# Performance work log

Measured on AMD Instinct MI355X. Metric: run time of the kernel, lower is better.

## Reference

```python
import jax, jax.numpy as jnp
import numpy as np
from jax import lax

I, H, O, S = 1024, 1024, 32000, 2048


def setup_inputs() -> dict:
    key = jax.random.key(0)
    ks = jax.random.split(key, 7)
    s = 1.0 / np.sqrt(H)
    return {
        "x": jax.random.normal(ks[0], (1, S, I), jnp.float32),
        "W_ih": jax.random.uniform(ks[1], (H, I), jnp.float32, -s, s),
        "W_hh": jax.random.uniform(ks[2], (H, H), jnp.float32, -s, s),
        "b_ih": jax.random.uniform(ks[3], (H,), jnp.float32, -s, s),
        "b_hh": jax.random.uniform(ks[4], (H,), jnp.float32, -s, s),
        "W_fc": jax.random.uniform(ks[5], (O, H), jnp.float32, -s, s),
        "b_fc": jax.random.uniform(ks[6], (O,), jnp.float32, -s, s),
    }


def reference(x, W_ih, W_hh, b_ih, b_hh, W_fc, b_fc):
    # Precompute input projection for all timesteps in one GEMM: [s, H]
    xp = jnp.einsum('si,hi->sh', x[0], W_ih) + b_ih + b_hh
    h0 = jnp.zeros((W_hh.shape[0],), x.dtype)

    def step(h, xt):
        h_new = jnp.tanh(xt + h @ W_hh.T)
        return h_new, h_new

    _, hs = lax.scan(step, h0, xp)  # hs: [s, H]
    # Linear head over all timesteps: [s, O]
    return hs @ W_fc.T + b_fc
```

## Files before the change

### kernel.cpp

```cpp
#include <hip/hip_runtime.h>
#include <math.h>

typedef _Float16 f16;
typedef f16 f16x2 __attribute__((ext_vector_type(2)));
typedef f16 f16x4 __attribute__((ext_vector_type(4)));
typedef f16 f16x8 __attribute__((ext_vector_type(8)));
typedef float f32x4 __attribute__((ext_vector_type(4)));

#define HDIM 1024
#define SEQ  2048
#define NBLK 16
#define NGWK 240
#define RPB  64
#define NTIL 4000

__global__ void k_clear(unsigned long long* __restrict__ p, int n,
                        unsigned* __restrict__ summ, int ns) {
  int stride = gridDim.x * blockDim.x;
  for (int i = blockIdx.x * blockDim.x + threadIdx.x; i < n; i += stride)
    p[i] = 0ULL;
  for (int i = blockIdx.x * blockDim.x + threadIdx.x; i < ns; i += stride)
    summ[i] = 0u;
}

__global__ void k_cvt(const float* __restrict__ in, f16* __restrict__ out, int n4) {
  int stride = gridDim.x * blockDim.x;
  for (int i = blockIdx.x * blockDim.x + threadIdx.x; i < n4; i += stride) {
    float4 v = ((const float4*)in)[i];
    f16x4 o = { (f16)v.x, (f16)v.y, (f16)v.z, (f16)v.w };
    ((f16x4*)out)[i] = o;
  }
}

__global__ void k_bias(const float* __restrict__ a, const float* __restrict__ b,
                       float* __restrict__ o) {
  int i = blockIdx.x * blockDim.x + threadIdx.x;
  if (i < HDIM) o[i] = a[i] + b[i];
}

__global__ __launch_bounds__(256) void k_gemm(
    const f16* __restrict__ A, const f16* __restrict__ B,
    const float* __restrict__ bias, float* __restrict__ C, int N)
{
  const int K = 1024;
  __shared__ __align__(16) f16 lsA[128 * 32];
  __shared__ __align__(16) f16 lsB[128 * 32];
  const int tid = threadIdx.x;
  const int l   = tid & 63;
  const int wv  = tid >> 6;
  const int mb  = blockIdx.y * 128;
  const int nb  = blockIdx.x * 128;
  const int wm  = (wv >> 1) * 64;
  const int wn  = (wv & 1) * 64;

  f32x4 acc[4][4] = {};

  for (int kt = 0; kt < K; kt += 32) {
    uint4 ra[2], rb[2];
#pragma unroll
    for (int i = 0; i < 2; ++i) {
      int c = tid + i * 256;
      int row = c >> 2, off = (c & 3) * 8;
      ra[i] = *(const uint4*)(A + (size_t)(mb + row) * K + kt + off);
      rb[i] = *(const uint4*)(B + (size_t)(nb + row) * K + kt + off);
    }
    __syncthreads();
#pragma unroll
    for (int i = 0; i < 2; ++i) {
      int c = tid + i * 256;
      *(uint4*)(lsA + c * 8) = ra[i];
      *(uint4*)(lsB + c * 8) = rb[i];
    }
    __syncthreads();

    f16x8 af[4], bf[4];
#pragma unroll
    for (int m = 0; m < 4; ++m)
      af[m] = *(const f16x8*)(lsA + (wm + m * 16 + (l & 15)) * 32 + (l >> 4) * 8);
#pragma unroll
    for (int n = 0; n < 4; ++n)
      bf[n] = *(const f16x8*)(lsB + (wn + n * 16 + (l & 15)) * 32 + (l >> 4) * 8);
#pragma unroll
    for (int m = 0; m < 4; ++m)
#pragma unroll
      for (int n = 0; n < 4; ++n)
        acc[m][n] = __builtin_amdgcn_mfma_f32_16x16x32_f16(af[m], bf[n], acc[m][n], 0, 0, 0);
  }

#pragma unroll
  for (int n = 0; n < 4; ++n) {
    int col = nb + wn + n * 16 + (l & 15);
    float bv = bias[col];
#pragma unroll
    for (int m = 0; m < 4; ++m) {
#pragma unroll
      for (int j = 0; j < 4; ++j) {
        int row = mb + wm + m * 16 + (l >> 4) * 4 + j;
        C[(size_t)row * N + col] = acc[m][n][j] + bv;
      }
    }
  }
}

__device__ __forceinline__ void pub64(unsigned long long* p, unsigned long long v) {
  (void)__hip_atomic_exchange(p, v, __ATOMIC_RELAXED, __HIP_MEMORY_SCOPE_AGENT);
}
__device__ __forceinline__ void pub32(unsigned* p, unsigned v) {
  (void)__hip_atomic_exchange(p, v, __ATOMIC_RELAXED, __HIP_MEMORY_SCOPE_AGENT);
}
__device__ __forceinline__ unsigned long long rd64(const unsigned long long* p) {
  return __hip_atomic_fetch_add((unsigned long long*)p, 0ULL,
                                __ATOMIC_RELAXED, __HIP_MEMORY_SCOPE_AGENT);
}
__device__ __forceinline__ unsigned rd32(const unsigned* p) {
  return __hip_atomic_fetch_add((unsigned*)p, 0u,
                                __ATOMIC_RELAXED, __HIP_MEMORY_SCOPE_AGENT);
}

__global__ __launch_bounds__(1024, 4) void k_main(
    const float* __restrict__ W,
    const float* __restrict__ xp,
    unsigned long long* __restrict__ pairs,
    unsigned* __restrict__ summ,
    f16* __restrict__ hs,
    const f16* __restrict__ Wfc,
    const float* __restrict__ bfc,
    float* __restrict__ out)
{
  __shared__ unsigned hl[544];
  __shared__ int s_dead;
  __shared__ __align__(16) f16 lsA[128 * 32];
  __shared__ __align__(16) f16 lsB[128 * 32];

  const int tid = threadIdx.x;
  const int l   = tid & 63;
  const int wv  = tid >> 6;

  if (blockIdx.x < NBLK) {
    const int b   = blockIdx.x;
    const int w   = wv;
    const int hfl = l >> 5;
    const int ch  = l & 31;
    const int r0  = b * RPB + w * 4 + hfl * 2;
    const int c0  = ch * 32;

    if (tid == 0) s_dead = 0;

    f16x2 wv0[16], wv1[16];
    {
      const float* w0 = W + (size_t)r0 * HDIM + c0;
      const float* w1 = w0 + HDIM;
#pragma unroll
      for (int j = 0; j < 16; ++j) {
        wv0[j] = f16x2{ (f16)w0[2 * j], (f16)w0[2 * j + 1] };
        wv1[j] = f16x2{ (f16)w1[2 * j], (f16)w1[2 * j + 1] };
      }
    }

    for (unsigned t = 1; t <= SEQ; ++t) {
      float x0 = 0.f, x1 = 0.f;
      if (ch == 0) {
        const float* xr = xp + (size_t)(t - 1) * HDIM + r0;
        x0 = xr[0]; x1 = xr[1];
      }

      if (w == 0) {
        const unsigned need = t - 1;
        {
          const unsigned* sp = summ + (size_t)(t - 1) * 16 + l;
          int g = 0;
          for (;;) {
            unsigned sv = need;
            if (l < 16) sv = rd32(sp);
            if (__ballot(sv != need) == 0ULL) break;
            if (++g > (1 << 20)) { if (l == 0) s_dead = 1; break; }
          }
        }
        {
          const unsigned long long* row = pairs + (size_t)(t - 1) * 512 + l * 8;
          unsigned long long u[8];
          int g = 0;
          for (;;) {
            bool ok = true;
#pragma unroll
            for (int j = 0; j < 8; ++j) u[j] = rd64(row + j);
#pragma unroll
            for (int j = 0; j < 8; ++j)
              ok &= ((unsigned)(u[j] >> 32) == (t - 1));
            if (__ballot(!ok) == 0ULL) break;
            if (++g > (1 << 20)) { if (l == 0) s_dead = 1; break; }
          }
          const int base = (l >> 1) * 17 + (l & 1) * 8;
#pragma unroll
          for (int j = 0; j < 8; ++j) hl[base + j] = (unsigned)u[j];
        }
      }
      __syncthreads();
      if (s_dead) return;

      float s0 = 0.f, s1 = 0.f;
#pragma unroll
      for (int j = 0; j < 16; ++j) {
        f16x2 hv = __builtin_bit_cast(f16x2, hl[ch * 17 + j]);
        s0 = __builtin_amdgcn_fdot2(wv0[j], hv, s0, false);
        s1 = __builtin_amdgcn_fdot2(wv1[j], hv, s1, false);
      }
#pragma unroll
      for (int m = 16; m >= 1; m >>= 1) {
        s0 += __shfl_xor(s0, m, 64);
        s1 += __shfl_xor(s1, m, 64);
      }

      if (ch == 0) {
        float a0 = x0 + s0, a1 = x1 + s1;
        float e0 = __expf(2.f * a0), e1 = __expf(2.f * a1);
        float h0 = 1.f - 2.f * __builtin_amdgcn_rcpf(e0 + 1.f);
        float h1 = 1.f - 2.f * __builtin_amdgcn_rcpf(e1 + 1.f);
        f16x2 hh = { (f16)h0, (f16)h1 };
        unsigned pay = __builtin_bit_cast(unsigned, hh);
        unsigned long long val = ((unsigned long long)t << 32) | (unsigned long long)pay;
        pub64(pairs + (size_t)t * 512 + (r0 >> 1), val);
        pub32((unsigned*)hs + (((size_t)t * HDIM + r0) >> 1), pay);
      }

      __syncthreads();
      if (tid == 0)
        pub32(summ + (size_t)t * 16 + b, t);
    }
    return;
  }

  const int g  = blockIdx.x - NBLK;
  const int wm = (wv >> 2) * 32;
  const int wn = (wv & 3) * 32;
  const int half = tid >> 9;
  const int i    = tid & 511;
  const int srow = i >> 2;
  const int soff = (i & 3) * 8;

  for (int ti = g; ti < NTIL; ti += NGWK) {
    const int mt = ti / 250, nt = ti % 250;
    const unsigned S = (unsigned)(mt * 128 + 128);

    if (wv == 0) {
      const unsigned* sp = summ + (size_t)S * 16 + l;
      int gu = 0;
      for (;;) {
        unsigned sv = S;
        if (l < 16) sv = rd32(sp);
        if (__ballot(sv < S) == 0ULL) break;
        __builtin_amdgcn_s_sleep(32);
        if (++gu > (1 << 21)) break;
      }
    }
    __syncthreads();

    const f16* A = hs + (size_t)(mt * 128 + 1) * HDIM;
    const f16* B = Wfc + (size_t)nt * 128 * HDIM;
    const f16* sbase = (half ? B : A) + (size_t)srow * HDIM + soff;

    f32x4 acc[2][2] = {};

    for (int kt = 0; kt < HDIM; kt += 32) {
      uint4 r = *(const uint4*)(sbase + kt);
      __syncthreads();
      *(uint4*)((half ? lsB : lsA) + i * 8) = r;
      __syncthreads();

      f16x8 af[2], bf[2];
#pragma unroll
      for (int m = 0; m < 2; ++m)
        af[m] = *(const f16x8*)(lsA + (wm + m * 16 + (l & 15)) * 32 + (l >> 4) * 8);
#pragma unroll
      for (int n = 0; n < 2; ++n)
        bf[n] = *(const f16x8*)(lsB + (wn + n * 16 + (l & 15)) * 32 + (l >> 4) * 8);
#pragma unroll
      for (int m = 0; m < 2; ++m)
#pragma unroll
        for (int n = 0; n < 2; ++n)
          acc[m][n] = __builtin_amdgcn_mfma_f32_16x16x32_f16(af[m], bf[n], acc[m][n], 0, 0, 0);
    }

#pragma unroll
    for (int n = 0; n < 2; ++n) {
      int col = nt * 128 + wn + n * 16 + (l & 15);
      float bv = bfc[col];
#pragma unroll
      for (int m = 0; m < 2; ++m) {
#pragma unroll
        for (int j = 0; j < 4; ++j) {
          int row = mt * 128 + wm + m * 16 + (l >> 4) * 4 + j;
          out[(size_t)row * 32000 + col] = acc[m][n][j] + bv;
        }
      }
    }
    __syncthreads();
  }
}

extern "C" void kernel_launch(void* const* d_in, const int* in_sizes, int n_in,
                              void* d_out, int out_size, void* d_ws, size_t ws_size,
                              hipStream_t stream) {
  const float* x    = (const float*)d_in[0];
  const float* W_ih = (const float*)d_in[1];
  const float* W_hh = (const float*)d_in[2];
  const float* b_ih = (const float*)d_in[3];
  const float* b_hh = (const float*)d_in[4];
  const float* W_fc = (const float*)d_in[5];
  const float* b_fc = (const float*)d_in[6];
  float* out = (float*)d_out;

  char* ws = (char*)d_ws;
  unsigned long long* pairs = (unsigned long long*)ws;
  f16*   hs16  = (f16*)(ws + 8500000);
  float* xp    = (float*)(ws + 12700000);
  f16*   x16   = (f16*)(ws + 21100000);
  f16*   wih16 = (f16*)(ws + 25300000);
  f16*   wfc16 = (f16*)(ws + 27400000);
  float* bsum  = (float*)(ws + 92936000);
  unsigned* summ = (unsigned*)(ws + 92940288);

  k_clear<<<1024, 256, 0, stream>>>(pairs, (SEQ + 1) * 512, summ, (SEQ + 1) * 16);
  k_cvt<<<1024, 256, 0, stream>>>(x, x16, 2048 * 1024 / 4);
  k_cvt<<<1024, 256, 0, stream>>>(W_ih, wih16, 1024 * 1024 / 4);
  k_cvt<<<2048, 256, 0, stream>>>(W_fc, wfc16, 32000 * 1024 / 4);
  k_bias<<<4, 256, 0, stream>>>(b_ih, b_hh, bsum);

  k_gemm<<<dim3(8, 16), 256, 0, stream>>>(x16, wih16, bsum, xp, 1024);

  k_main<<<NBLK + NGWK, 1024, 0, stream>>>(W_hh, xp, pairs, summ, hs16,
                                           wfc16, b_fc, out);
}
```

Measured before the change: 4.725 ms.

## Replace summary-flag wait with per-block double-buffered push mailboxes

Each recurrence block now pushes its tagged hidden-state words into a private, double-buffered mailbox for every one of the 16 recurrent blocks. It no longer writes one shared per-timestep row that readers gate behind a separate summary-flag poll. Consumers poll only their own mailbox slot and check the step tag, which removes one serial polling phase from each of the 2048 dependent steps and shrinks the cleared buffer. In exchange, each producer lane issues 16 atomic stores per step. Correctness now relies on the step dependency to keep a slot from being overwritten before it is read.

```diff
diff --git a/kernel.cpp b/kernel.cpp
--- a/kernel.cpp
+++ b/kernel.cpp
@@ -120,7 +120,7 @@
 __global__ __launch_bounds__(1024, 4) void k_main(
     const float* __restrict__ W,
     const float* __restrict__ xp,
-    unsigned long long* __restrict__ pairs,
+    unsigned long long* __restrict__ mbox,
     unsigned* __restrict__ summ,
     f16* __restrict__ hs,
     const f16* __restrict__ Wfc,
@@ -143,6 +143,7 @@
     const int ch  = l & 31;
     const int r0  = b * RPB + w * 4 + hfl * 2;
     const int c0  = ch * 32;
+    const int wd  = r0 >> 1;
 
     if (tid == 0) s_dead = 0;
 
@@ -165,35 +166,24 @@
       }
 
       if (w == 0) {
+        const int sl = (int)((t - 1) & 1);
+        const unsigned long long* row = mbox + ((size_t)b * 2 + sl) * 512 + l * 8;
         const unsigned need = t - 1;
-        {
-          const unsigned* sp = summ + (size_t)(t - 1) * 16 + l;
-          int g = 0;
-          for (;;) {
-            unsigned sv = need;
-            if (l < 16) sv = rd32(sp);
-            if (__ballot(sv != need) == 0ULL) break;
-            if (++g > (1 << 20)) { if (l == 0) s_dead = 1; break; }
-          }
+        unsigned long long u[8];
+        int g = 0;
+        for (;;) {
+          bool ok = true;
+#pragma unroll
+          for (int j = 0; j < 8; ++j) u[j] = rd64(row + j);
+#pragma unroll
+          for (int j = 0; j < 8; ++j)
+            ok &= ((unsigned)(u[j] >> 32) == need);
+          if (__ballot(!ok) == 0ULL) break;
+          if (++g > (1 << 20)) { if (l == 0) s_dead = 1; break; }
         }
-        {
-          const unsigned long long* row = pairs + (size_t)(t - 1) * 512 + l * 8;
-          unsigned long long u[8];
-          int g = 0;
-          for (;;) {
-            bool ok = true;
-#pragma unroll
-            for (int j = 0; j < 8; ++j) u[j] = rd64(row + j);
-#pragma unroll
-            for (int j = 0; j < 8; ++j)
-              ok &= ((unsigned)(u[j] >> 32) == (t - 1));
-            if (__ballot(!ok) == 0ULL) break;
-            if (++g > (1 << 20)) { if (l == 0) s_dead = 1; break; }
-          }
-          const int base = (l >> 1) * 17 + (l & 1) * 8;
-#pragma unroll
-          for (int j = 0; j < 8; ++j) hl[base + j] = (unsigned)u[j];
-        }
+        const int base = (l >> 1) * 17 + (l & 1) * 8;
+#pragma unroll
+        for (int j = 0; j < 8; ++j) hl[base + j] = (unsigned)u[j];
       }
       __syncthreads();
       if (s_dead) return;
@@ -219,7 +209,12 @@
         f16x2 hh = { (f16)h0, (f16)h1 };
         unsigned pay = __builtin_bit_cast(unsigned, hh);
         unsigned long long val = ((unsigned long long)t << 32) | (unsigned long long)pay;
-        pub64(pairs + (size_t)t * 512 + (r0 >> 1), val);
+        const int sl = (int)(t & 1);
+#pragma unroll
+        for (int cc = 0; cc < NBLK; ++cc) {
+          int c = (cc + b) & (NBLK - 1);
+          pub64(mbox + ((size_t)c * 2 + sl) * 512 + wd, val);
+        }
         pub32((unsigned*)hs + (((size_t)t * HDIM + r0) >> 1), pay);
       }
 
@@ -311,7 +306,7 @@
   float* out = (float*)d_out;
 
   char* ws = (char*)d_ws;
-  unsigned long long* pairs = (unsigned long long*)ws;
+  unsigned long long* mbox = (unsigned long long*)ws;
   f16*   hs16  = (f16*)(ws + 8500000);
   float* xp    = (float*)(ws + 12700000);
   f16*   x16   = (f16*)(ws + 21100000);
@@ -320,7 +315,7 @@
   float* bsum  = (float*)(ws + 92936000);
   unsigned* summ = (unsigned*)(ws + 92940288);
 
-  k_clear<<<1024, 256, 0, stream>>>(pairs, (SEQ + 1) * 512, summ, (SEQ + 1) * 16);
+  k_clear<<<256, 256, 0, stream>>>(mbox, NBLK * 2 * 512, summ, (SEQ + 1) * 16);
   k_cvt<<<1024, 256, 0, stream>>>(x, x16, 2048 * 1024 / 4);
   k_cvt<<<1024, 256, 0, stream>>>(W_ih, wih16, 1024 * 1024 / 4);
   k_cvt<<<2048, 256, 0, stream>>>(W_fc, wfc16, 32000 * 1024 / 4);
@@ -328,6 +323,6 @@
 
   k_gemm<<<dim3(8, 16), 256, 0, stream>>>(x16, wih16, bsum, xp, 1024);
 
-  k_main<<<NBLK + NGWK, 1024, 0, stream>>>(W_hh, xp, pairs, summ, hs16,
+  k_main<<<NBLK + NGWK, 1024, 0, stream>>>(W_hh, xp, mbox, summ, hs16,
                                            wfc16, b_fc, out);
 }
```

After: 6.760 ms. 43.1% more time.

## Double-buffer recurrence exchange and use fixed per-block progress flags

Applied to the files above, without the earlier changes.

The per-timestep hidden-state exchange buffer shrinks from one row per step to two ping-pong rows. The recurrence blocks now poll a small set of fixed, 128-byte-padded progress counters instead of a fresh flag row for every step. A separate per-step flag array is kept for the output-GEMM workers, so they still wait on the timestep they need. The aim is to cut the synchronization latency of each serial step by polling the same hot L2 lines, and to shrink the workspace and the clearing work. The trade-off is that buffer reuse now depends on the monotonic-counter ordering, and repeated writes to the same lines could add coherence contention.

```diff
diff --git a/kernel.cpp b/kernel.cpp
--- a/kernel.cpp
+++ b/kernel.cpp
@@ -15,12 +15,13 @@
 #define NTIL 4000
 
 __global__ void k_clear(unsigned long long* __restrict__ p, int n,
-                        unsigned* __restrict__ summ, int ns) {
+                        unsigned* __restrict__ sR, int nr,
+                        unsigned* __restrict__ sG, int ng) {
   int stride = gridDim.x * blockDim.x;
-  for (int i = blockIdx.x * blockDim.x + threadIdx.x; i < n; i += stride)
-    p[i] = 0ULL;
-  for (int i = blockIdx.x * blockDim.x + threadIdx.x; i < ns; i += stride)
-    summ[i] = 0u;
+  int id = blockIdx.x * blockDim.x + threadIdx.x;
+  for (int i = id; i < n; i += stride) p[i] = 0ULL;
+  for (int i = id; i < nr; i += stride) sR[i] = 0u;
+  for (int i = id; i < ng; i += stride) sG[i] = 0u;
 }
 
 __global__ void k_cvt(const float* __restrict__ in, f16* __restrict__ out, int n4) {
@@ -121,7 +122,8 @@
     const float* __restrict__ W,
     const float* __restrict__ xp,
     unsigned long long* __restrict__ pairs,
-    unsigned* __restrict__ summ,
+    unsigned* __restrict__ sumR,
+    unsigned* __restrict__ sumG,
     f16* __restrict__ hs,
     const f16* __restrict__ Wfc,
     const float* __restrict__ bfc,
@@ -167,17 +169,16 @@
       if (w == 0) {
         const unsigned need = t - 1;
         {
-          const unsigned* sp = summ + (size_t)(t - 1) * 16 + l;
           int g = 0;
           for (;;) {
             unsigned sv = need;
-            if (l < 16) sv = rd32(sp);
-            if (__ballot(sv != need) == 0ULL) break;
+            if (l < 16) sv = rd32(sumR + l * 32);
+            if (__ballot(sv < need) == 0ULL) break;
             if (++g > (1 << 20)) { if (l == 0) s_dead = 1; break; }
           }
         }
         {
-          const unsigned long long* row = pairs + (size_t)(t - 1) * 512 + l * 8;
+          const unsigned long long* row = pairs + ((t - 1) & 1) * 512 + l * 8;
           unsigned long long u[8];
           int g = 0;
           for (;;) {
@@ -219,13 +220,15 @@
         f16x2 hh = { (f16)h0, (f16)h1 };
         unsigned pay = __builtin_bit_cast(unsigned, hh);
         unsigned long long val = ((unsigned long long)t << 32) | (unsigned long long)pay;
-        pub64(pairs + (size_t)t * 512 + (r0 >> 1), val);
+        pub64(pairs + (t & 1) * 512 + (r0 >> 1), val);
         pub32((unsigned*)hs + (((size_t)t * HDIM + r0) >> 1), pay);
       }
 
       __syncthreads();
-      if (tid == 0)
-        pub32(summ + (size_t)t * 16 + b, t);
+      if (tid == 0) {
+        pub32(sumR + b * 32, t);
+        pub32(sumG + (size_t)t * 16 + b, t);
+      }
     }
     return;
   }
@@ -243,7 +246,7 @@
     const unsigned S = (unsigned)(mt * 128 + 128);
 
     if (wv == 0) {
-      const unsigned* sp = summ + (size_t)S * 16 + l;
+      const unsigned* sp = sumG + (size_t)S * 16 + l;
       int gu = 0;
       for (;;) {
         unsigned sv = S;
@@ -312,15 +315,17 @@
 
   char* ws = (char*)d_ws;
   unsigned long long* pairs = (unsigned long long*)ws;
-  f16*   hs16  = (f16*)(ws + 8500000);
-  float* xp    = (float*)(ws + 12700000);
-  f16*   x16   = (f16*)(ws + 21100000);
-  f16*   wih16 = (f16*)(ws + 25300000);
-  f16*   wfc16 = (f16*)(ws + 27400000);
-  float* bsum  = (float*)(ws + 92936000);
-  unsigned* summ = (unsigned*)(ws + 92940288);
-
-  k_clear<<<1024, 256, 0, stream>>>(pairs, (SEQ + 1) * 512, summ, (SEQ + 1) * 16);
+  unsigned* sumR  = (unsigned*)(ws + 8192);
+  unsigned* sumG  = (unsigned*)(ws + 10240);
+  f16*   hs16  = (f16*)(ws + 141376);
+  float* xp    = (float*)(ws + 4337728);
+  f16*   x16   = (f16*)(ws + 12726336);
+  f16*   wih16 = (f16*)(ws + 16920640);
+  f16*   wfc16 = (f16*)(ws + 19017792);
+  float* bsum  = (float*)(ws + 84553792);
+
+  k_clear<<<256, 256, 0, stream>>>(pairs, 2 * 512, sumR, 16 * 32,
+                                   sumG, (SEQ + 1) * 16);
   k_cvt<<<1024, 256, 0, stream>>>(x, x16, 2048 * 1024 / 4);
   k_cvt<<<1024, 256, 0, stream>>>(W_ih, wih16, 1024 * 1024 / 4);
   k_cvt<<<2048, 256, 0, stream>>>(W_fc, wfc16, 32000 * 1024 / 4);
@@ -328,6 +333,6 @@
 
   k_gemm<<<dim3(8, 16), 256, 0, stream>>>(x16, wih16, bsum, xp, 1024);
 
-  k_main<<<NBLK + NGWK, 1024, 0, stream>>>(W_hh, xp, pairs, summ, hs16,
+  k_main<<<NBLK + NGWK, 1024, 0, stream>>>(W_hh, xp, pairs, sumR, sumG, hs16,
                                            wfc16, b_fc, out);
 }
```

Measured after the change: 4.643 ms. About the same (-1.7%).
